# Optimization experiments

Measured on AMD Instinct MI355X. Metric: run time of the kernel, lower is better.

## Reference

```python
import jax, jax.numpy as jnp
import numpy as np

B, C, H, W = 4, 256, 64, 64
HEADS, GROUPS = 8, 8
HEAD_DIM = C // HEADS
EPS_GN = 1e-5
EPS_NORM = 1e-12


def group_norm(x, gamma, beta):
    b, c, h, w = x.shape
    xr = x.reshape(b, GROUPS, c // GROUPS, h, w)
    mean = xr.mean(axis=(2, 3, 4), keepdims=True)
    var = xr.var(axis=(2, 3, 4), keepdims=True)
    xn = ((xr - mean) / jnp.sqrt(var + EPS_GN)).reshape(b, c, h, w)
    return xn * gamma[None, :, None, None] + beta[None, :, None, None]


def conv1x1(x, w):
    # w: (C_out, C_in) pointwise conv
    return jnp.einsum('oc,bchw->bohw', w, x)


def dwconv3x3(x, w, b):
    # depthwise 3x3, w: (C, 1, 3, 3)
    y = jax.lax.conv_general_dilated(
        x, w, window_strides=(1, 1), padding='SAME',
        dimension_numbers=('NCHW', 'OIHW', 'NCHW'),
        feature_group_count=C)
    return y + b[None, :, None, None]


def setup_inputs() -> dict:
    key = jax.random.key(0)
    ks = jax.random.split(key, 7)
    s = 0.05
    f32 = jnp.float32
    return {
        'x': jax.random.normal(ks[0], (B, C, H, W), f32),
        'wq': jax.random.normal(ks[1], (C, C), f32) * s,
        'gq_gamma': jnp.ones((C,), f32), 'gq_beta': jnp.zeros((C,), f32),
        'wk': jax.random.normal(ks[2], (C, C), f32) * s,
        'gk_gamma': jnp.ones((C,), f32), 'gk_beta': jnp.zeros((C,), f32),
        'wv': jax.random.normal(ks[3], (C, C), f32) * s,
        'wp': jax.random.normal(ks[4], (C, C), f32) * s,
        'bp': jnp.zeros((C,), f32),
        'gp_gamma': jnp.ones((C,), f32), 'gp_beta': jnp.zeros((C,), f32),
        'dw1': jax.random.normal(ks[5], (C, 1, 3, 3), f32) * s,
        'db1': jnp.zeros((C,), f32),
        'dw2': jax.random.normal(ks[6], (C, 1, 3, 3), f32) * s,
        'db2': jnp.zeros((C,), f32),
    }


def reference(x, wq, gq_gamma, gq_beta, wk, gk_gamma, gk_beta, wv,
              wp, bp, gp_gamma, gp_beta, dw1, db1, dw2, db2):
    b, c, h, w = x.shape
    q = group_norm(conv1x1(x, wq), gq_gamma, gq_beta)
    k = group_norm(conv1x1(x, wk), gk_gamma, gk_beta)
    v = conv1x1(x, wv)

    def to_tokens(t):
        # (B,C,H,W) -> (B*H*W, heads, head_dim)
        return t.transpose(0, 2, 3, 1).reshape(b * h * w, HEADS, HEAD_DIM)

    q, k, v = to_tokens(q), to_tokens(k), to_tokens(v)
    qn = q / jnp.maximum(jnp.linalg.norm(q, axis=-1, keepdims=True), EPS_NORM)
    kn = k / jnp.maximum(jnp.linalg.norm(k, axis=-1, keepdims=True), EPS_NORM)
    scale = 1.0 / np.sqrt(HEAD_DIM).astype(np.float32)
    # per-pixel spectral attention: (N, heads, d, d)
    attn = jnp.einsum('nhd,nhe->nhde', qn, kn) * scale
    attn = jax.nn.softmax(attn, axis=-1)
    out = jnp.einsum('nhde,nhe->nhd', attn, v)
    out = out.reshape(b, h, w, c).transpose(0, 3, 1, 2)

    pos = dwconv3x3(x, dw1, db1)
    pos = jax.nn.gelu(pos, approximate=False)
    pos = dwconv3x3(pos, dw2, db2)

    out = out + pos
    out = conv1x1(out, wp) + bp[None, :, None, None]
    out = group_norm(out, gp_gamma, gp_beta)
    return out
```

## Files before the change

### kernel.cpp

```cpp
#include <hip/hip_runtime.h>
#include <math.h>
#include <stdint.h>

#define C_ 256
#define HW_ 4096
#define PLANE (C_*HW_)
#define INV_CNT (1.f / 131072.f)
#define NSLOT 16

typedef __attribute__((ext_vector_type(8))) short bf16x8;
typedef __attribute__((ext_vector_type(4))) float f32x4;

__device__ __forceinline__ unsigned short f2bf(float f) {
    union { float f; unsigned int u; } v; v.f = f;
    unsigned int r = v.u + 0x7fffu + ((v.u >> 16) & 1u);
    return (unsigned short)(r >> 16);
}

__device__ __forceinline__ void load_lds16(const void* g, void* l) {
    __builtin_amdgcn_global_load_lds(
        (const __attribute__((address_space(1))) unsigned int*)g,
        (__attribute__((address_space(3))) unsigned int*)l, 16, 0, 0);
}

__global__ __launch_bounds__(256) void wcvt_kernel(
    const float* __restrict__ wq, const float* __restrict__ wk,
    const float* __restrict__ wv, const float* __restrict__ wp,
    unsigned short* __restrict__ dst, float* __restrict__ stats)
{
    int idx = blockIdx.x * 256 + threadIdx.x;
    const float* s = (idx < 65536) ? wq : (idx < 131072) ? wk
                   : (idx < 196608) ? wv : wp;
    dst[idx] = f2bf(s[idx & 65535]);
    if (blockIdx.x == 0) {
#pragma unroll
        for (int i = 0; i < 12; i++) stats[threadIdx.x + i * 256] = 0.f;
    }
}

__global__ __launch_bounds__(256) void transpose_cvt_kernel(
    const float* __restrict__ src, unsigned short* __restrict__ dst)
{
    __shared__ float tile[64][65];
    int b = blockIdx.z;
    const float* s = src + (size_t)b * PLANE;
    unsigned short* d = dst + (size_t)b * PLANE;
    int c0 = blockIdx.y * 64, n0 = blockIdx.x * 64;
    int t = threadIdx.x;
    int r = t >> 6, col = t & 63;
#pragma unroll
    for (int i = 0; i < 16; i++)
        tile[r + i * 4][col] = s[(size_t)(c0 + r + i * 4) * HW_ + n0 + col];
    __syncthreads();
#pragma unroll
    for (int i = 0; i < 16; i++)
        d[(size_t)(n0 + r + i * 4) * 256 + c0 + col] = f2bf(tile[col][r + i * 4]);
}

__global__ __launch_bounds__(256) void transpose_cvt_add_kernel(
    const float* __restrict__ pos, const unsigned short* __restrict__ attn,
    unsigned short* __restrict__ dst)
{
    __shared__ float tile[64][65];
    int b = blockIdx.z;
    const float* s = pos + (size_t)b * PLANE;
    const unsigned short* a = attn + (size_t)b * PLANE;
    unsigned short* d = dst + (size_t)b * PLANE;
    int c0 = blockIdx.y * 64, n0 = blockIdx.x * 64;
    int t = threadIdx.x;
    int r = t >> 6, col = t & 63;
#pragma unroll
    for (int i = 0; i < 16; i++)
        tile[r + i * 4][col] = s[(size_t)(c0 + r + i * 4) * HW_ + n0 + col];
    __syncthreads();
#pragma unroll
    for (int i = 0; i < 16; i++) {
        size_t o = (size_t)(n0 + r + i * 4) * 256 + c0 + col;
        float av = __uint_as_float(((unsigned)a[o]) << 16);
        d[o] = f2bf(tile[col][r + i * 4] + av);
    }
}

__device__ __forceinline__ void mfma_core(
    const unsigned short* __restrict__ A,
    const unsigned short* __restrict__ Bm,
    int m0, int n0, f32x4 (&acc)[4][4])
{
    __shared__ unsigned short As[128 * 32];
    __shared__ unsigned short Bs[128 * 32];
    const int t = threadIdx.x;
    const int lane = t & 63, wave = t >> 6;

#pragma unroll
    for (int i = 0; i < 4; i++)
#pragma unroll
        for (int j = 0; j < 4; j++) acc[i][j] = (f32x4)0.f;

    const int srow = wave * 32 + (lane >> 2);
    const int scol = (lane & 3) * 8;
    const unsigned short* ga = A  + (size_t)(m0 + srow) * 256 + scol;
    const unsigned short* gb = Bm + (size_t)(n0 + srow) * 256 + scol;
    unsigned short* la = As + (wave * 32) * 32;
    unsigned short* lb = Bs + (wave * 32) * 32;

    const int wm = wave >> 1, wn = wave & 1;
    const int fr = lane & 15, kg = lane >> 4;

    for (int k0 = 0; k0 < 256; k0 += 32) {
        if (k0) __syncthreads();
        load_lds16(ga + k0,             la);
        load_lds16(ga + k0 + 16 * 256,  la + 16 * 32);
        load_lds16(gb + k0,             lb);
        load_lds16(gb + k0 + 16 * 256,  lb + 16 * 32);
        __syncthreads();

        bf16x8 af[4], bfr[4];
#pragma unroll
        for (int i = 0; i < 4; i++) {
            af[i]  = *(const bf16x8*)(As + (wm * 64 + i * 16 + fr) * 32 + kg * 8);
            bfr[i] = *(const bf16x8*)(Bs + (wn * 64 + i * 16 + fr) * 32 + kg * 8);
        }
#pragma unroll
        for (int mi = 0; mi < 4; mi++)
#pragma unroll
            for (int ni = 0; ni < 4; ni++)
                acc[mi][ni] = __builtin_amdgcn_mfma_f32_16x16x32_bf16(
                    af[mi], bfr[ni], acc[mi][ni], 0, 0, 0);
    }
}

__device__ __forceinline__ void stat_atomic(
    float s0, float ss0, float s1, float ss1, float* d0, float* d1)
{
#pragma unroll
    for (int off = 32; off >= 1; off >>= 1) {
        s0  += __shfl_down(s0, off);  ss0 += __shfl_down(ss0, off);
        s1  += __shfl_down(s1, off);  ss1 += __shfl_down(ss1, off);
    }
    if ((threadIdx.x & 63) == 0) {
        atomicAdd(d0, s0); atomicAdd(d0 + 1, ss0);
        atomicAdd(d1, s1); atomicAdd(d1 + 1, ss1);
    }
}

__device__ __forceinline__ void stat_read(const float* sp, float& S, float& SS) {
    S = 0.f; SS = 0.f;
#pragma unroll
    for (int i = 0; i < NSLOT; i++) { S += sp[i * 2]; SS += sp[i * 2 + 1]; }
}

__global__ __launch_bounds__(256) void gemm_qkv_mfma(
    const unsigned short* __restrict__ wbf, const unsigned short* __restrict__ xT,
    unsigned short* __restrict__ q, unsigned short* __restrict__ k,
    unsigned short* __restrict__ v, float* __restrict__ stats)
{
    int z = blockIdx.z;
    int batch = z & 3, which = z >> 2;
    unsigned short* Y = ((which == 0) ? q : (which == 1) ? k : v)
                        + (size_t)batch * PLANE;
    const unsigned short* A  = wbf + which * 65536;
    const unsigned short* Bm = xT + (size_t)batch * PLANE;
    const int m0 = blockIdx.x * 128;
    const int n0 = blockIdx.y * 128;

    f32x4 acc[4][4];
    mfma_core(A, Bm, m0, n0, acc);

    const int lane = threadIdx.x & 63, wave = threadIdx.x >> 6;
    const int wm = wave >> 1, wn = wave & 1;
    const int cl = lane & 15, qd = lane >> 4;

    if (which < 2) {
        float s[2] = {0.f, 0.f}, ss[2] = {0.f, 0.f};
#pragma unroll
        for (int mi = 0; mi < 4; mi++)
#pragma unroll
            for (int ni = 0; ni < 4; ni++)
#pragma unroll
                for (int r = 0; r < 4; r++) {
                    float vv = acc[mi][ni][r];
                    s[mi >> 1] += vv; ss[mi >> 1] += vv * vv;
                }
        int g0 = (m0 >> 5) + wm * 2;
        int slot = blockIdx.y & (NSLOT - 1);
        float* d0 = stats + (size_t)(which * 32 + batch * 8 + g0) * (NSLOT * 2) + slot * 2;
        stat_atomic(s[0], ss[0], s[1], ss[1], d0, d0 + NSLOT * 2);
    }

#pragma unroll
    for (int mi = 0; mi < 4; mi++) {
        int oc = m0 + wm * 64 + mi * 16 + qd * 4;
#pragma unroll
        for (int ni = 0; ni < 4; ni++) {
            int token = n0 + wn * 64 + ni * 16 + cl;
            uint2 pk;
            pk.x = (unsigned)f2bf(acc[mi][ni][0]) | ((unsigned)f2bf(acc[mi][ni][1]) << 16);
            pk.y = (unsigned)f2bf(acc[mi][ni][2]) | ((unsigned)f2bf(acc[mi][ni][3]) << 16);
            *(uint2*)&Y[(size_t)token * 256 + oc] = pk;
        }
    }
}

__global__ __launch_bounds__(256) void gemm_out_mfma(
    const unsigned short* __restrict__ wbf, const unsigned short* __restrict__ aT,
    const float* __restrict__ bp, float* __restrict__ y, float* __restrict__ stats)
{
    int batch = blockIdx.z;
    const unsigned short* A  = aT + (size_t)batch * PLANE;
    const unsigned short* Bm = wbf + 3 * 65536;
    float* Y = y + (size_t)batch * PLANE;
    const int m0 = blockIdx.x * 128;
    const int n0 = blockIdx.y * 128;

    f32x4 acc[4][4];
    mfma_core(A, Bm, m0, n0, acc);

    const int lane = threadIdx.x & 63, wave = threadIdx.x >> 6;
    const int wm = wave >> 1, wn = wave & 1;
    const int cl = lane & 15, qd = lane >> 4;

    float s[2] = {0.f, 0.f}, ss[2] = {0.f, 0.f};
#pragma unroll
    for (int ni = 0; ni < 4; ni++) {
        int oc = n0 + wn * 64 + ni * 16 + cl;
        float bb = bp[oc];
#pragma unroll
        for (int mi = 0; mi < 4; mi++) {
            int tk = m0 + wm * 64 + mi * 16 + qd * 4;
            float4 o;
            o.x = acc[mi][ni][0] + bb; o.y = acc[mi][ni][1] + bb;
            o.z = acc[mi][ni][2] + bb; o.w = acc[mi][ni][3] + bb;
            s[ni >> 1] += o.x + o.y + o.z + o.w;
            ss[ni >> 1] += o.x * o.x + o.y * o.y + o.z * o.z + o.w * o.w;
            *(float4*)&Y[(size_t)oc * HW_ + tk] = o;
        }
    }
    int g0 = (n0 >> 5) + wn * 2;
    int slot = blockIdx.x & (NSLOT - 1);
    float* d0 = stats + (size_t)(64 + batch * 8 + g0) * (NSLOT * 2) + slot * 2;
    stat_atomic(s[0], ss[0], s[1], ss[1], d0, d0 + NSLOT * 2);
}

__device__ __forceinline__ void bf16x32_load(const unsigned short* p, float* o) {
    const uint4* u4 = (const uint4*)p;
#pragma unroll
    for (int i = 0; i < 4; i++) {
        uint4 u = u4[i];
        o[i*8+0] = __uint_as_float(u.x << 16); o[i*8+1] = __uint_as_float(u.x & 0xffff0000u);
        o[i*8+2] = __uint_as_float(u.y << 16); o[i*8+3] = __uint_as_float(u.y & 0xffff0000u);
        o[i*8+4] = __uint_as_float(u.z << 16); o[i*8+5] = __uint_as_float(u.z & 0xffff0000u);
        o[i*8+6] = __uint_as_float(u.w << 16); o[i*8+7] = __uint_as_float(u.w & 0xffff0000u);
    }
}

__global__ __launch_bounds__(256) void attn_tok_kernel(
    const unsigned short* __restrict__ qtok, const unsigned short* __restrict__ ktok,
    const unsigned short* __restrict__ vtok, const float* __restrict__ stats,
    const float* __restrict__ gqg, const float* __restrict__ gqb,
    const float* __restrict__ gkg, const float* __restrict__ gkb,
    unsigned short* __restrict__ out)
{
    __shared__ float sqg[256], sqb[256], skg[256], skb[256];
    const int t = threadIdx.x;
    sqg[t] = gqg[t]; sqb[t] = gqb[t]; skg[t] = gkg[t]; skb[t] = gkb[t];
    __syncthreads();

    const int h = t & 7;
    const int pix = blockIdx.x * 32 + (t >> 3);
    const int b = pix >> 12;
    const size_t base = (size_t)pix * 256 + h * 32;
    const float K2 = 0.17677669529663687f * 1.4426950408889634f;

    float a[32], kn[32], vv[32];

    {
        float S, SS;
        stat_read(stats + (size_t)(b * 8 + h) * (NSLOT * 2), S, SS);
        float m = S * INV_CNT;
        float r = rsqrtf(SS * INV_CNT - m * m + 1e-5f);
        float qv[32], ssum = 0.f;
        bf16x32_load(qtok + base, qv);
#pragma unroll
        for (int j = 0; j < 32; j++) {
            float g = r * sqg[h * 32 + j];
            qv[j] = (qv[j] - m) * g + sqb[h * 32 + j];
            ssum = fmaf(qv[j], qv[j], ssum);
        }
        float inv = K2 / fmaxf(sqrtf(ssum), 1e-12f);
#pragma unroll
        for (int j = 0; j < 32; j++) a[j] = qv[j] * inv;
    }
    {
        float S, SS;
        stat_read(stats + (size_t)(32 + b * 8 + h) * (NSLOT * 2), S, SS);
        float m = S * INV_CNT;
        float r = rsqrtf(SS * INV_CNT - m * m + 1e-5f);
        float ssum = 0.f;
        bf16x32_load(ktok + base, kn);
#pragma unroll
        for (int j = 0; j < 32; j++) {
            float g = r * skg[h * 32 + j];
            kn[j] = (kn[j] - m) * g + skb[h * 32 + j];
            ssum = fmaf(kn[j], kn[j], ssum);
        }
        float inv = 1.f / fmaxf(sqrtf(ssum), 1e-12f);
#pragma unroll
        for (int j = 0; j < 32; j++) kn[j] *= inv;
    }
    bf16x32_load(vtok + base, vv);

    uint4* op = (uint4*)(out + base);
#pragma unroll
    for (int di = 0; di < 4; di++) {
        unsigned int od[4];
#pragma unroll
        for (int dp = 0; dp < 4; dp++) {
            float o2[2];
#pragma unroll
            for (int dd = 0; dd < 2; dd++) {
                float ad = a[di * 8 + dp * 2 + dd];
                float num = 0.f, den = 0.f;
#pragma unroll
                for (int e = 0; e < 32; e++) {
                    float w = __builtin_amdgcn_exp2f(ad * kn[e]);
                    num = fmaf(w, vv[e], num);
                    den += w;
                }
                o2[dd] = num / den;
            }
            od[dp] = (unsigned)f2bf(o2[0]) | ((unsigned)f2bf(o2[1]) << 16);
        }
        op[di] = make_uint4(od[0], od[1], od[2], od[3]);
    }
}

__device__ __forceinline__ float gelu_exact(float v) {
    return 0.5f * v * (1.f + erff(v * 0.70710678118654752f));
}

__global__ __launch_bounds__(256) void dwconv_fused_kernel(
    const float* __restrict__ x,
    const float* __restrict__ dw1, const float* __restrict__ db1,
    const float* __restrict__ dw2, const float* __restrict__ db2,
    float* __restrict__ pos)
{
    __shared__ float xs[66 * 68];
    __shared__ float ps[66 * 68];
    const int bc = blockIdx.x;
    const int c = bc & 255;
    const int t = threadIdx.x;
    const float* plane = x + (size_t)bc * 4096;

    float w1[9], w2[9];
#pragma unroll
    for (int i = 0; i < 9; i++) { w1[i] = dw1[c * 9 + i]; w2[i] = dw2[c * 9 + i]; }
    const float b1 = db1[c], b2 = db2[c];

    for (int i = t; i < 66 * 66; i += 256) {
        int r = i / 66, cc = i - r * 66;
        int gr = r - 1, gc = cc - 1;
        float v = 0.f;
        if ((unsigned)gr < 64u && (unsigned)gc < 64u) v = plane[gr * 64 + gc];
        xs[r * 68 + cc] = v;
    }
    __syncthreads();

    for (int i = t; i < 66 * 66; i += 256) {
        int pr = i / 66, pc = i - pr * 66;
        int gr = pr - 1, gc = pc - 1;
        float val = 0.f;
        if ((unsigned)gr < 64u && (unsigned)gc < 64u) {
            float s = b1;
#pragma unroll
            for (int ky = 0; ky < 3; ky++)
#pragma unroll
                for (int kx = 0; kx < 3; kx++)
                    s += w1[ky * 3 + kx] * xs[(gr + ky) * 68 + (gc + kx)];
            val = gelu_exact(s);
        }
        ps[pr * 68 + pc] = val;
    }
    __syncthreads();

    for (int i = t; i < 4096; i += 256) {
        int orow = i >> 6, ocol = i & 63;
        float s = b2;
#pragma unroll
        for (int ky = 0; ky < 3; ky++)
#pragma unroll
            for (int kx = 0; kx < 3; kx++)
                s += w2[ky * 3 + kx] * ps[(orow + ky) * 68 + (ocol + kx)];
        pos[(size_t)bc * 4096 + i] = s;
    }
}

__global__ __launch_bounds__(256) void gn_apply_kernel(
    float* __restrict__ y, const float* __restrict__ stats,
    const float* __restrict__ gamma, const float* __restrict__ beta)
{
    int i4 = blockIdx.x * 256 + threadIdx.x;
    int idx = i4 * 4;
    int c = (idx >> 12) & 255;
    int bg = ((idx >> 20) << 3) | (c >> 5);
    float S, SS;
    stat_read(stats + (size_t)(64 + bg) * (NSLOT * 2), S, SS);
    float mean = S * INV_CNT;
    float rstd = rsqrtf(SS * INV_CNT - mean * mean + 1e-5f);
    float ga = rstd * gamma[c], be = beta[c] - mean * ga;
    float4 v4 = *(float4*)&y[idx];
    v4.x = v4.x * ga + be;
    v4.y = v4.y * ga + be;
    v4.z = v4.z * ga + be;
    v4.w = v4.w * ga + be;
    *(float4*)&y[idx] = v4;
}

extern "C" void kernel_launch(void* const* d_in, const int* in_sizes, int n_in,
                              void* d_out, int out_size, void* d_ws, size_t ws_size,
                              hipStream_t stream)
{
    const float* x   = (const float*)d_in[0];
    const float* wq  = (const float*)d_in[1];
    const float* gqg = (const float*)d_in[2];
    const float* gqb = (const float*)d_in[3];
    const float* wk  = (const float*)d_in[4];
    const float* gkg = (const float*)d_in[5];
    const float* gkb = (const float*)d_in[6];
    const float* wv  = (const float*)d_in[7];
    const float* wp  = (const float*)d_in[8];
    const float* bp  = (const float*)d_in[9];
    const float* gpg = (const float*)d_in[10];
    const float* gpb = (const float*)d_in[11];
    const float* dw1 = (const float*)d_in[12];
    const float* db1 = (const float*)d_in[13];
    const float* dw2 = (const float*)d_in[14];
    const float* db2 = (const float*)d_in[15];
    float* out = (float*)d_out;

    char* ws = (char*)d_ws;
    const size_t MB8 = (size_t)8 * 1024 * 1024;
    unsigned short* qtok = (unsigned short*)(ws);
    unsigned short* ktok = (unsigned short*)(ws + MB8);
    unsigned short* vtok = (unsigned short*)(ws + 2 * MB8);
    unsigned short* atok = (unsigned short*)(ws + 3 * MB8);
    unsigned short* xT   = (unsigned short*)(ws + 4 * MB8);
    unsigned short* aT   = xT;
    float*          pos  = (float*)(ws);
    unsigned short* wbf  = (unsigned short*)(ws + 5 * MB8);
    float*          stats= (float*)(ws + 5 * MB8 + 524288);

    dim3 blk(256);
    wcvt_kernel<<<dim3(1024), blk, 0, stream>>>(wq, wk, wv, wp, wbf, stats);
    transpose_cvt_kernel<<<dim3(64, 4, 4), blk, 0, stream>>>(x, xT);
    gemm_qkv_mfma<<<dim3(2, 32, 12), blk, 0, stream>>>(wbf, xT, qtok, ktok, vtok, stats);
    attn_tok_kernel<<<dim3(512), blk, 0, stream>>>(qtok, ktok, vtok, stats,
                                                   gqg, gqb, gkg, gkb, atok);
    dwconv_fused_kernel<<<dim3(1024), blk, 0, stream>>>(x, dw1, db1, dw2, db2, pos);
    transpose_cvt_add_kernel<<<dim3(64, 4, 4), blk, 0, stream>>>(pos, atok, aT);
    gemm_out_mfma<<<dim3(32, 2, 4), blk, 0, stream>>>(wbf, aT, bp, out, stats);
    gn_apply_kernel<<<dim3(4096), blk, 0, stream>>>(out, stats, gpg, gpb);
}
```

Measured before the change: 183.0 us.

## Fuse weight conversion into transpose, store pos as bf16, deepen GEMM K-step

Merges the weight bf16 conversion and stats zeroing into the input transpose kernel, removing one launch. The depthwise-conv output is stored as bf16 in the qtok buffer instead of fp32, which halves its write and read traffic at the cost of extra rounding before the add. The GEMM core now loads two 32-wide K slices per barrier into doubled LDS buffers, halving the number of synchronisations. The larger LDS footprint may reduce occupancy.

```diff
diff --git a/kernel.cpp b/kernel.cpp
--- a/kernel.cpp
+++ b/kernel.cpp
@@ -17,36 +17,41 @@
     return (unsigned short)(r >> 16);
 }
 
+__device__ __forceinline__ float bf2f(unsigned short u) {
+    return __uint_as_float(((unsigned)u) << 16);
+}
+
 __device__ __forceinline__ void load_lds16(const void* g, void* l) {
     __builtin_amdgcn_global_load_lds(
         (const __attribute__((address_space(1))) unsigned int*)g,
         (__attribute__((address_space(3))) unsigned int*)l, 16, 0, 0);
 }
 
-__global__ __launch_bounds__(256) void wcvt_kernel(
+__global__ __launch_bounds__(256) void transpose_cvt_kernel(
+    const float* __restrict__ src, unsigned short* __restrict__ dst,
     const float* __restrict__ wq, const float* __restrict__ wk,
     const float* __restrict__ wv, const float* __restrict__ wp,
-    unsigned short* __restrict__ dst, float* __restrict__ stats)
-{
-    int idx = blockIdx.x * 256 + threadIdx.x;
-    const float* s = (idx < 65536) ? wq : (idx < 131072) ? wk
-                   : (idx < 196608) ? wv : wp;
-    dst[idx] = f2bf(s[idx & 65535]);
-    if (blockIdx.x == 0) {
-#pragma unroll
-        for (int i = 0; i < 12; i++) stats[threadIdx.x + i * 256] = 0.f;
-    }
-}
-
-__global__ __launch_bounds__(256) void transpose_cvt_kernel(
-    const float* __restrict__ src, unsigned short* __restrict__ dst)
+    unsigned short* __restrict__ wbf, float* __restrict__ stats)
 {
     __shared__ float tile[64][65];
+    int t = threadIdx.x;
+
+    int bid = blockIdx.x + 64 * (blockIdx.y + 4 * blockIdx.z);
+    {
+        int widx = bid * 256 + t;
+        const float* s = (widx < 65536) ? wq : (widx < 131072) ? wk
+                       : (widx < 196608) ? wv : wp;
+        wbf[widx] = f2bf(s[widx & 65535]);
+        if (bid == 0) {
+#pragma unroll
+            for (int i = 0; i < 12; i++) stats[t + i * 256] = 0.f;
+        }
+    }
+
     int b = blockIdx.z;
     const float* s = src + (size_t)b * PLANE;
     unsigned short* d = dst + (size_t)b * PLANE;
     int c0 = blockIdx.y * 64, n0 = blockIdx.x * 64;
-    int t = threadIdx.x;
     int r = t >> 6, col = t & 63;
 #pragma unroll
     for (int i = 0; i < 16; i++)
@@ -58,12 +63,12 @@
 }
 
 __global__ __launch_bounds__(256) void transpose_cvt_add_kernel(
-    const float* __restrict__ pos, const unsigned short* __restrict__ attn,
+    const unsigned short* __restrict__ pos, const unsigned short* __restrict__ attn,
     unsigned short* __restrict__ dst)
 {
     __shared__ float tile[64][65];
     int b = blockIdx.z;
-    const float* s = pos + (size_t)b * PLANE;
+    const unsigned short* s = pos + (size_t)b * PLANE;
     const unsigned short* a = attn + (size_t)b * PLANE;
     unsigned short* d = dst + (size_t)b * PLANE;
     int c0 = blockIdx.y * 64, n0 = blockIdx.x * 64;
@@ -71,13 +76,12 @@
     int r = t >> 6, col = t & 63;
 #pragma unroll
     for (int i = 0; i < 16; i++)
-        tile[r + i * 4][col] = s[(size_t)(c0 + r + i * 4) * HW_ + n0 + col];
+        tile[r + i * 4][col] = bf2f(s[(size_t)(c0 + r + i * 4) * HW_ + n0 + col]);
     __syncthreads();
 #pragma unroll
     for (int i = 0; i < 16; i++) {
         size_t o = (size_t)(n0 + r + i * 4) * 256 + c0 + col;
-        float av = __uint_as_float(((unsigned)a[o]) << 16);
-        d[o] = f2bf(tile[col][r + i * 4] + av);
+        d[o] = f2bf(tile[col][r + i * 4] + bf2f(a[o]));
     }
 }
 
@@ -86,8 +90,8 @@
     const unsigned short* __restrict__ Bm,
     int m0, int n0, f32x4 (&acc)[4][4])
 {
-    __shared__ unsigned short As[128 * 32];
-    __shared__ unsigned short Bs[128 * 32];
+    __shared__ unsigned short As[2][128 * 32];
+    __shared__ unsigned short Bs[2][128 * 32];
     const int t = threadIdx.x;
     const int lane = t & 63, wave = t >> 6;
 
@@ -100,32 +104,38 @@
     const int scol = (lane & 3) * 8;
     const unsigned short* ga = A  + (size_t)(m0 + srow) * 256 + scol;
     const unsigned short* gb = Bm + (size_t)(n0 + srow) * 256 + scol;
-    unsigned short* la = As + (wave * 32) * 32;
-    unsigned short* lb = Bs + (wave * 32) * 32;
+    const int lbase = (wave * 32) * 32;
 
     const int wm = wave >> 1, wn = wave & 1;
     const int fr = lane & 15, kg = lane >> 4;
 
-    for (int k0 = 0; k0 < 256; k0 += 32) {
+    for (int k0 = 0; k0 < 256; k0 += 64) {
         if (k0) __syncthreads();
-        load_lds16(ga + k0,             la);
-        load_lds16(ga + k0 + 16 * 256,  la + 16 * 32);
-        load_lds16(gb + k0,             lb);
-        load_lds16(gb + k0 + 16 * 256,  lb + 16 * 32);
+        load_lds16(ga + k0,            As[0] + lbase);
+        load_lds16(ga + k0 + 16 * 256, As[0] + lbase + 16 * 32);
+        load_lds16(gb + k0,            Bs[0] + lbase);
+        load_lds16(gb + k0 + 16 * 256, Bs[0] + lbase + 16 * 32);
+        load_lds16(ga + k0 + 32,            As[1] + lbase);
+        load_lds16(ga + k0 + 32 + 16 * 256, As[1] + lbase + 16 * 32);
+        load_lds16(gb + k0 + 32,            Bs[1] + lbase);
+        load_lds16(gb + k0 + 32 + 16 * 256, Bs[1] + lbase + 16 * 32);
         __syncthreads();
 
-        bf16x8 af[4], bfr[4];
-#pragma unroll
-        for (int i = 0; i < 4; i++) {
-            af[i]  = *(const bf16x8*)(As + (wm * 64 + i * 16 + fr) * 32 + kg * 8);
-            bfr[i] = *(const bf16x8*)(Bs + (wn * 64 + i * 16 + fr) * 32 + kg * 8);
-        }
-#pragma unroll
-        for (int mi = 0; mi < 4; mi++)
-#pragma unroll
-            for (int ni = 0; ni < 4; ni++)
-                acc[mi][ni] = __builtin_amdgcn_mfma_f32_16x16x32_bf16(
-                    af[mi], bfr[ni], acc[mi][ni], 0, 0, 0);
+#pragma unroll
+        for (int kk = 0; kk < 2; kk++) {
+            bf16x8 af[4], bfr[4];
+#pragma unroll
+            for (int i = 0; i < 4; i++) {
+                af[i]  = *(const bf16x8*)(As[kk] + (wm * 64 + i * 16 + fr) * 32 + kg * 8);
+                bfr[i] = *(const bf16x8*)(Bs[kk] + (wn * 64 + i * 16 + fr) * 32 + kg * 8);
+            }
+#pragma unroll
+            for (int mi = 0; mi < 4; mi++)
+#pragma unroll
+                for (int ni = 0; ni < 4; ni++)
+                    acc[mi][ni] = __builtin_amdgcn_mfma_f32_16x16x32_bf16(
+                        af[mi], bfr[ni], acc[mi][ni], 0, 0, 0);
+        }
     }
 }
 
@@ -342,7 +352,7 @@
     const float* __restrict__ x,
     const float* __restrict__ dw1, const float* __restrict__ db1,
     const float* __restrict__ dw2, const float* __restrict__ db2,
-    float* __restrict__ pos)
+    unsigned short* __restrict__ pos)
 {
     __shared__ float xs[66 * 68];
     __shared__ float ps[66 * 68];
@@ -390,7 +400,7 @@
 #pragma unroll
             for (int kx = 0; kx < 3; kx++)
                 s += w2[ky * 3 + kx] * ps[(orow + ky) * 68 + (ocol + kx)];
-        pos[(size_t)bc * 4096 + i] = s;
+        pos[(size_t)bc * 4096 + i] = f2bf(s);
     }
 }
 
@@ -445,13 +455,12 @@
     unsigned short* atok = (unsigned short*)(ws + 3 * MB8);
     unsigned short* xT   = (unsigned short*)(ws + 4 * MB8);
     unsigned short* aT   = xT;
-    float*          pos  = (float*)(ws);
+    unsigned short* pos  = qtok;
     unsigned short* wbf  = (unsigned short*)(ws + 5 * MB8);
     float*          stats= (float*)(ws + 5 * MB8 + 524288);
 
     dim3 blk(256);
-    wcvt_kernel<<<dim3(1024), blk, 0, stream>>>(wq, wk, wv, wp, wbf, stats);
-    transpose_cvt_kernel<<<dim3(64, 4, 4), blk, 0, stream>>>(x, xT);
+    transpose_cvt_kernel<<<dim3(64, 4, 4), blk, 0, stream>>>(x, xT, wq, wk, wv, wp, wbf, stats);
     gemm_qkv_mfma<<<dim3(2, 32, 12), blk, 0, stream>>>(wbf, xT, qtok, ktok, vtok, stats);
     attn_tok_kernel<<<dim3(512), blk, 0, stream>>>(qtok, ktok, vtok, stats,
                                                    gqg, gqb, gkg, gkb, atok);
```

Measured after the change: 177.9 us. 1.03x faster.
